# Performance work log

Measured on AMD Instinct MI355X. Metric: run time of the kernel, lower is better.

The kernel has to match this reference:

```python
import jax, jax.numpy as jnp
import numpy as np
import math
from jax.scipy.special import gammaln, logsumexp

N, D, K = 262144, 16, 64
K_TRUE = 32
TAU = 0.1
LOG2PI = math.log(2.0 * math.pi)


def setup_inputs() -> dict:
    key = jax.random.key(0)
    k0, k1, k2, k3, k4, k5 = jax.random.split(key, 6)
    # data locations, scaled so log(r_scale_met) > 0 (Gamma rate positivity, as in original init)
    met_locs = jax.random.normal(k0, (N, D), dtype=jnp.float32) * 20.0
    R = met_locs.max(0) - met_locs.min(0)  # per-dim range, diag of Ro
    r_scale = jnp.sqrt(jnp.sum(R ** 2)) / (2.0 * K_TRUE)
    mu = jax.random.normal(k1, (K, D), dtype=jnp.float32) * jnp.sqrt(R)[None, :]  # MVN(0, Ro)
    pi = jax.random.dirichlet(k2, jnp.full((K,), 1.0 / K, dtype=jnp.float32)).astype(jnp.float32)
    # log of Gamma(0.5, rate=0.5) sample; clipped for numerical safety of the setup draw
    lambda_mu = jnp.clip(jnp.log(jax.random.gamma(k3, 0.5, (D,)) / 0.5), -3.0, 3.0).astype(jnp.float32)
    b = jax.random.normal(k4, (K, D), dtype=jnp.float32)
    C = jnp.full((K,), jnp.log(r_scale), dtype=jnp.float32)
    r = jnp.full((K,), jnp.log(r_scale), dtype=jnp.float32)
    z = jax.random.normal(k5, (N, K), dtype=jnp.float32)
    return {"met_locs": met_locs, "mu": mu, "pi": pi, "lambda_mu": lambda_mu,
            "b": b, "C": C, "r": r, "z": z}


def reference(met_locs, mu, pi, lambda_mu, b, C, r, z):
    Df = float(D)
    R = met_locs.max(0) - met_locs.min(0)                      # diag of Ro
    c = 1.25 + (D - 1) / 4.0
    g = 0.25 + (D - 1) / 4.0
    G = c / (50.0 * g) * jnp.sqrt(jnp.sum(R ** 2))

    # ---- z_loss: Concrete prior on z_act + Concrete-weighted Gaussian mixture ----
    logz = jax.nn.log_softmax(z, axis=1)                       # log z_act, [N, K]
    logpi = jax.nn.log_softmax(pi)                             # [K]
    # isotropic Gaussian log N(x_m; mu_k, exp(r_k) I) without [N,K,D] intermediate
    sq = ((met_locs ** 2).sum(1, keepdims=True)
          - 2.0 * met_locs @ mu.T
          + (mu ** 2).sum(1)[None, :])                          # [N, K]
    logN = -0.5 * sq / jnp.exp(r)[None, :] - 0.5 * Df * (r + LOG2PI)[None, :]
    mix = logsumexp(logz + logN, axis=1)                       # log sum_k z_mk N_k(x_m)
    # Concrete (Gumbel-softmax) log-density at y = z_act with probs softmax(pi), temp TAU
    t = logpi[None, :] - TAU * logz                            # [N, K]
    con = (gammaln(float(K)) + (K - 1) * math.log(TAU)
           + jnp.sum(logpi) - (TAU + 1.0) * logz.sum(1)
           - K * logsumexp(t, axis=1))                          # [N]
    z_loss = -(con + mix).sum()

    # ---- pi_loss: Dirichlet(1/K) prior (up to const) ----
    pi_loss = -((1.0 / K - 1.0) * logpi).sum()

    # ---- mu_loss: MVN(b, Lambda Ro Lambda) with Lambda = diag(lambda_mu) ----
    var_mu = (lambda_mu ** 2) * R                              # diag of Bo, [D]
    mu_lp = (-0.5 * (((mu - b) ** 2) / var_mu[None, :]).sum(1)
             - 0.5 * jnp.log(var_mu).sum() - 0.5 * Df * LOG2PI)
    mu_loss = -mu_lp.sum()

    # ---- lambda_loss: Gamma(0.5, 0.5) on exp(lambda_mu) ----
    lam_lp = (0.5 * math.log(0.5) - gammaln(0.5)
              + (0.5 - 1.0) * lambda_mu - 0.5 * jnp.exp(lambda_mu))
    lambda_loss = -lam_lp.sum()

    # ---- b_loss: standard normal MVN ----
    b_loss = 0.5 * (b ** 2).sum() + 0.5 * K * Df * LOG2PI

    # ---- r_loss: Gamma(c, rate=C) on 1/exp(r) ----
    r_lp = c * jnp.log(C) + (c - 1.0) * (-r) - C * jnp.exp(-r) - gammaln(c)
    r_loss = -r_lp.sum()

    # ---- C_loss: Gamma(g, rate=G) on 1/exp(C) ----
    C_lp = g * jnp.log(G) + (g - 1.0) * (-C) - G * jnp.exp(-C) - gammaln(g)
    C_loss = -C_lp.sum()

    # forward sums in self.learn order: r, mu, z, pi, b, lambda, C
    return r_loss + mu_loss + z_loss + pi_loss + b_loss + lambda_loss + C_loss
```

## Files before the change

kernel.cpp:

```cpp
#include <hip/hip_runtime.h>
#include <math.h>

#define NROWS 262144
#define NBLK  1024
#define NTHR  256
#define LOG2PI_F 1.8378770664093453f
#define L2E_F   1.4426950408889634f
#define LN2_F   0.6931471805599453f

#define EXP2F(x) __builtin_amdgcn_exp2f(x)
#define LOG2F(x) __builtin_amdgcn_logf(x)

#define WS_ZS   1024
#define WS_MN   2048
#define WS_MX   18432
#define WS_CONS 34816

template<int CTRL>
__device__ __forceinline__ float dppf(float x){
  return __int_as_float(__builtin_amdgcn_update_dpp(0, __float_as_int(x), CTRL, 0xF, 0xF, true));
}
__device__ __forceinline__ float rl63(float x){
  return __int_as_float(__builtin_amdgcn_readlane(__float_as_int(x), 63));
}
__device__ __forceinline__ float wsum(float x){
  x += dppf<0x111>(x); x += dppf<0x112>(x); x += dppf<0x114>(x); x += dppf<0x118>(x);
  x += dppf<0x142>(x); x += dppf<0x143>(x);
  return rl63(x);
}

__global__ void setup_k(const float* __restrict__ mu, const float* __restrict__ pi,
                        const float* __restrict__ rr, float* __restrict__ ws){
  int k = threadIdx.x;
  float pik = pi[k], rk = rr[k];
  float mumu = 0.f;
  #pragma unroll
  for (int d = 0; d < 16; ++d){ float m = mu[k*16+d]; mumu = fmaf(m, m, mumu); }
  float lse_pi = __logf(wsum(__expf(pik)));
  float lpk = pik - lse_pi;
  float ir = __expf(-rk), Bk = -0.5f*ir;
  float Dk = fmaf(Bk, mumu, -8.f*(rk + LOG2PI_F));
  float* cons = ws + WS_CONS;
  cons[k*4+0] = __expf(lpk);
  cons[k*4+1] = ir*L2E_F;
  cons[k*4+2] = Dk*L2E_F;
  cons[k*4+3] = Bk*L2E_F;
}

__global__ __launch_bounds__(NTHR, 4)
void zmain(const float* __restrict__ met, const float* __restrict__ mu,
           const float* __restrict__ z, float* __restrict__ ws)
{
  __shared__ float zt[4][2112];
  const int tid = threadIdx.x, lane = tid & 63, wid = tid >> 6;
  const int bx = blockIdx.x;

  float pmn[4], pmx[4];
  #pragma unroll
  for (int j=0;j<4;++j){ pmn[j]=INFINITY; pmx[j]=-INFINITY; }
  {
    const float4* mb = (const float4*)(met + (size_t)bx*4096);
    #pragma unroll
    for (int i=0;i<4;++i){
      float4 v = mb[i*256 + tid];
      pmn[0]=fminf(pmn[0],v.x); pmx[0]=fmaxf(pmx[0],v.x);
      pmn[1]=fminf(pmn[1],v.y); pmx[1]=fmaxf(pmx[1],v.y);
      pmn[2]=fminf(pmn[2],v.z); pmx[2]=fmaxf(pmx[2],v.z);
      pmn[3]=fminf(pmn[3],v.w); pmx[3]=fmaxf(pmx[3],v.w);
    }
  }

  const int rbw = bx*256 + wid*64;
  const float4* xr = (const float4*)(met + (size_t)(rbw + lane)*16);
  float4 xa = xr[0], xb = xr[1], xc = xr[2], xd = xr[3];
  float xx = 0.f;
  xx=fmaf(xa.x,xa.x,xx); xx=fmaf(xa.y,xa.y,xx); xx=fmaf(xa.z,xa.z,xx); xx=fmaf(xa.w,xa.w,xx);
  xx=fmaf(xb.x,xb.x,xx); xx=fmaf(xb.y,xb.y,xx); xx=fmaf(xb.z,xb.z,xx); xx=fmaf(xb.w,xb.w,xx);
  xx=fmaf(xc.x,xc.x,xx); xx=fmaf(xc.y,xc.y,xx); xx=fmaf(xc.z,xc.z,xx); xx=fmaf(xc.w,xc.w,xx);
  xx=fmaf(xd.x,xd.x,xx); xx=fmaf(xd.y,xd.y,xx); xx=fmaf(xd.z,xd.z,xx); xx=fmaf(xd.w,xd.w,xx);

  const float4* z4 = (const float4*)z;
  const int g8 = lane >> 3, c8 = lane & 7;
  float4 sA[8], sB[8];
  #pragma unroll
  for (int j=0;j<8;++j) sA[j] = z4[(size_t)(rbw + j*8 + g8)*16 + c8];
  #pragma unroll
  for (int j=0;j<8;++j) sB[j] = z4[(size_t)(rbw + j*8 + g8)*16 + 8 + c8];
  #pragma unroll
  for (int j=0;j<8;++j){
    int b = (j*8+g8)*33 + c8*4;
    zt[wid][b]=sA[j].x; zt[wid][b+1]=sA[j].y; zt[wid][b+2]=sA[j].z; zt[wid][b+3]=sA[j].w;
  }

  const float4* cons4 = (const float4*)(ws + WS_CONS);
  const float4* mu4   = (const float4*)mu;

  float sez=0.f, seu=0.f, sea=0.f, m2=-1e30f, szA=0.f;

#define STEPK(K) { \
    float4 cc = cons4[K]; \
    float4 M0 = mu4[(K)*4+0], M1 = mu4[(K)*4+1], M2v = mu4[(K)*4+2], M3 = mu4[(K)*4+3]; \
    float zkv = zt[wid][lane*33 + ((K)&31)]; \
    float zk2 = zkv*L2E_F; \
    szA += zkv; \
    sez += EXP2F(zk2); \
    seu = fmaf(cc.x, EXP2F(-0.1f*zk2), seu); \
    float dt = 0.f; \
    dt=fmaf(xa.x,M0.x,dt); dt=fmaf(xa.y,M0.y,dt); dt=fmaf(xa.z,M0.z,dt); dt=fmaf(xa.w,M0.w,dt); \
    dt=fmaf(xb.x,M1.x,dt); dt=fmaf(xb.y,M1.y,dt); dt=fmaf(xb.z,M1.z,dt); dt=fmaf(xb.w,M1.w,dt); \
    dt=fmaf(xc.x,M2v.x,dt); dt=fmaf(xc.y,M2v.y,dt); dt=fmaf(xc.z,M2v.z,dt); dt=fmaf(xc.w,M2v.w,dt); \
    dt=fmaf(xd.x,M3.x,dt); dt=fmaf(xd.y,M3.y,dt); dt=fmaf(xd.z,M3.z,dt); dt=fmaf(xd.w,M3.w,dt); \
    float t1  = fmaf(cc.w, xx, zk2); \
    float av2 = fmaf(cc.y, dt, t1) + cc.z; \
    float d2 = av2 - m2; \
    float ee = EXP2F(-fabsf(d2)); \
    bool fl = d2 > 0.f; \
    sea = fmaf(sea, fl?ee:1.f, fl?1.f:ee); \
    m2 = fmaxf(m2, av2); }

  #pragma unroll 4
  for (int kk=0; kk<32; ++kk) STEPK(kk)

  #pragma unroll
  for (int j=0;j<8;++j){
    int b = (j*8+g8)*33 + c8*4;
    zt[wid][b]=sB[j].x; zt[wid][b+1]=sB[j].y; zt[wid][b+2]=sB[j].z; zt[wid][b+3]=sB[j].w;
  }
  #pragma unroll 4
  for (int kk=32; kk<64; ++kk) STEPK(kk)
#undef STEPK

  float l2sez = LOG2F(sez), l2seu = LOG2F(seu), l2sea = LOG2F(sea);
  float accA = LN2_F * (fmaf(63.f, l2sez, m2 + l2sea) - 64.f*l2seu);

  __syncthreads();
  float* scr = &zt[0][0];
  float wa = wsum(accA), wz = wsum(szA);
  if (lane == 0){ scr[2112 + wid] = wa; scr[2120 + wid] = wz; }
  #pragma unroll
  for (int j=0;j<4;++j){
    int d = (4*tid + j) & 15;
    scr[       d*66 + (tid>>2)] = pmn[j];
    scr[1056 + d*66 + (tid>>2)] = pmx[j];
  }
  __syncthreads();
  if (tid == 0){
    ws[bx]         = scr[2112]+scr[2113]+scr[2114]+scr[2115];
    ws[WS_ZS + bx] = scr[2120]+scr[2121]+scr[2122]+scr[2123];
  }
  if (tid < 16){
    float mnv = INFINITY, mxv = -INFINITY;
    for (int c2=0;c2<64;++c2){
      mnv = fminf(mnv, scr[tid*66+c2]);
      mxv = fmaxf(mxv, scr[1056+tid*66+c2]);
    }
    ws[WS_MN + bx*16 + tid] = mnv;
    ws[WS_MX + bx*16 + tid] = mxv;
  }
}

__global__ __launch_bounds__(NTHR)
void fin_k(const float* __restrict__ mu, const float* __restrict__ pi,
           const float* __restrict__ lam, const float* __restrict__ bp,
           const float* __restrict__ Cv,  const float* __restrict__ rr,
           const float* __restrict__ ws,  float* __restrict__ out,
           float cgam, float lamconst, float lg_c, float lg_g)
{
  __shared__ double sda[NTHR], sdz[NTHR];
  __shared__ float smn[16][66], smx[16][66];
  __shared__ float Rfin[16], vars[16];
  const int tid = threadIdx.x;

  {
    const float4* wa4 = (const float4*)ws;
    const float4* wz4 = (const float4*)(ws + WS_ZS);
    float4 a = wa4[tid], zz = wz4[tid];
    sda[tid] = (double)a.x + (double)a.y + (double)a.z + (double)a.w;
    sdz[tid] = (double)zz.x + (double)zz.y + (double)zz.z + (double)zz.w;
  }
  float pmn[4], pmx[4];
  #pragma unroll
  for (int j=0;j<4;++j){ pmn[j]=INFINITY; pmx[j]=-INFINITY; }
  {
    const float4* mn4 = (const float4*)(ws + WS_MN);
    const float4* mx4 = (const float4*)(ws + WS_MX);
    #pragma unroll
    for (int i=0;i<16;++i){
      float4 v = mn4[i*256 + tid];
      pmn[0]=fminf(pmn[0],v.x); pmn[1]=fminf(pmn[1],v.y);
      pmn[2]=fminf(pmn[2],v.z); pmn[3]=fminf(pmn[3],v.w);
      float4 w = mx4[i*256 + tid];
      pmx[0]=fmaxf(pmx[0],w.x); pmx[1]=fmaxf(pmx[1],w.y);
      pmx[2]=fmaxf(pmx[2],w.z); pmx[3]=fmaxf(pmx[3],w.w);
    }
  }
  #pragma unroll
  for (int j=0;j<4;++j){
    int d = (4*tid + j) & 15;
    smn[d][tid>>2] = pmn[j];
    smx[d][tid>>2] = pmx[j];
  }
  __syncthreads();
  for (int s = NTHR/2; s > 0; s >>= 1){
    if (tid < s){ sda[tid] += sda[tid+s]; sdz[tid] += sdz[tid+s]; }
    __syncthreads();
  }
  if (tid < 16){
    float mnv = INFINITY, mxv = -INFINITY;
    for (int c2=0;c2<64;++c2){ mnv = fminf(mnv, smn[tid][c2]); mxv = fmaxf(mxv, smx[tid][c2]); }
    float Rd = mxv - mnv;
    Rfin[tid] = Rd;
    float l = lam[tid];
    vars[tid] = l*l*Rd;
  }
  __syncthreads();

  if (tid < 64){
    int kk = tid;
    float sumR2 = 0.f;
    #pragma unroll
    for (int dd = 0; dd < 16; ++dd) sumR2 = fmaf(Rfin[dd], Rfin[dd], sumR2);
    float G = 0.025f * sqrtf(sumR2);

    float pik2 = pi[kk];
    float sp   = wsum(pik2);
    float lse2 = __logf(wsum(__expf(pik2)));
    float slogpi = sp - 64.f*lse2;

    float qsum = 0.f, slv = 0.f, bb = 0.f;
    #pragma unroll
    for (int dd = 0; dd < 16; ++dd){
      float df = mu[kk*16+dd] - bp[kk*16+dd];
      qsum += df*df / vars[dd];
      slv  += __logf(vars[dd]);
      float bv = bp[kk*16+dd];
      bb = fmaf(bv, bv, bb);
    }
    float mu_term = 0.5f*qsum + 0.5f*slv + 8.0f*LOG2PI_F;
    float rk2 = rr[kk], Ck = Cv[kk];
    float r_lp = 5.f*__logf(Ck) - 4.f*rk2 - Ck*__expf(-rk2) - lg_c;
    float C_lp = 4.f*__logf(G)  - 3.f*Ck  - G*__expf(-Ck)  - lg_g;
    float lam_term = 0.f;
    if (kk < 16){ float l = lam[kk]; lam_term = lamconst - 0.5f*l - 0.5f*__expf(l); }

    float per = mu_term + 0.5f*bb - r_lp - C_lp - lam_term;
    float persum = wsum(per);

    if (kk == 0){
      double zpart = sda[0] + 262144.0*(double)(cgam + slogpi) - 1.1*sdz[0];
      double tot = (double)persum
                 + (1.0 - 1.0/64.0)*(double)slogpi
                 + 512.0*(double)LOG2PI_F
                 - zpart;
      out[0] = (float)tot;
    }
  }
}

extern "C" void kernel_launch(void* const* d_in, const int* in_sizes, int n_in,
                              void* d_out, int out_size, void* d_ws, size_t ws_size,
                              hipStream_t stream) {
  const float* met = (const float*)d_in[0];
  const float* mu  = (const float*)d_in[1];
  const float* pi  = (const float*)d_in[2];
  const float* lam = (const float*)d_in[3];
  const float* bpp = (const float*)d_in[4];
  const float* Cv  = (const float*)d_in[5];
  const float* rr  = (const float*)d_in[6];
  const float* zz  = (const float*)d_in[7];
  float* out = (float*)d_out;
  float* ws  = (float*)d_ws;

  float cgam     = (float)(lgamma(64.0) + 63.0*log(0.1));
  float lamconst = (float)(0.5*log(0.5) - lgamma(0.5));
  float lg_c     = (float)lgamma(5.0);
  float lg_g     = (float)lgamma(4.0);

  setup_k<<<dim3(1), dim3(64), 0, stream>>>(mu, pi, rr, ws);
  zmain<<<dim3(NBLK), dim3(NTHR), 0, stream>>>(met, mu, zz, ws);
  fin_k<<<dim3(1), dim3(NTHR), 0, stream>>>(mu, pi, lam, bpp, Cv, rr, ws, out,
                                            cgam, lamconst, lg_c, lg_g);
}
```

Baseline: 131.5 us.

## Split K across wave pairs with direct z loads and LDS merge

Each row is now handled by two waves, each covering half of the 64 mixture components. Each wave reads its z values directly as float4 from its own row, replacing the LDS transpose staging. The partial max, sum and log-sum-exp states are merged through shared memory using a rescaled log-sum-exp combine. The block count doubles, launch bounds target higher occupancy, and the final reduction reads twice as many partials. This trades less per-thread serial work and no z transpose for uncoalesced per-row z loads and an extra barrier and merge step.

```diff
diff --git a/kernel.cpp b/kernel.cpp
--- a/kernel.cpp
+++ b/kernel.cpp
@@ -2,7 +2,7 @@
 #include <math.h>
 
 #define NROWS 262144
-#define NBLK  1024
+#define NBLK  2048
 #define NTHR  256
 #define LOG2PI_F 1.8378770664093453f
 #define L2E_F   1.4426950408889634f
@@ -11,10 +11,10 @@
 #define EXP2F(x) __builtin_amdgcn_exp2f(x)
 #define LOG2F(x) __builtin_amdgcn_logf(x)
 
-#define WS_ZS   1024
-#define WS_MN   2048
-#define WS_MX   18432
-#define WS_CONS 34816
+#define WS_ZS   2048
+#define WS_MN   4096
+#define WS_MX   36864
+#define WS_CONS 69632
 
 template<int CTRL>
 __device__ __forceinline__ float dppf(float x){
@@ -47,21 +47,24 @@
   cons[k*4+3] = Bk*L2E_F;
 }
 
-__global__ __launch_bounds__(NTHR, 4)
+__global__ __launch_bounds__(NTHR, 8)
 void zmain(const float* __restrict__ met, const float* __restrict__ mu,
            const float* __restrict__ z, float* __restrict__ ws)
 {
-  __shared__ float zt[4][2112];
+  __shared__ float mrg[2][64][6];
+  __shared__ float scr[2116];
   const int tid = threadIdx.x, lane = tid & 63, wid = tid >> 6;
+  const int pair = wid >> 1, kh = wid & 1;
   const int bx = blockIdx.x;
+  const int r = bx*128 + pair*64 + lane;
 
   float pmn[4], pmx[4];
   #pragma unroll
   for (int j=0;j<4;++j){ pmn[j]=INFINITY; pmx[j]=-INFINITY; }
   {
-    const float4* mb = (const float4*)(met + (size_t)bx*4096);
-    #pragma unroll
-    for (int i=0;i<4;++i){
+    const float4* mb = (const float4*)(met + (size_t)bx*2048);
+    #pragma unroll
+    for (int i=0;i<2;++i){
       float4 v = mb[i*256 + tid];
       pmn[0]=fminf(pmn[0],v.x); pmx[0]=fmaxf(pmx[0],v.x);
       pmn[1]=fminf(pmn[1],v.y); pmx[1]=fmaxf(pmx[1],v.y);
@@ -70,8 +73,7 @@
     }
   }
 
-  const int rbw = bx*256 + wid*64;
-  const float4* xr = (const float4*)(met + (size_t)(rbw + lane)*16);
+  const float4* xr = (const float4*)(met + (size_t)r*16);
   float4 xa = xr[0], xb = xr[1], xc = xr[2], xd = xr[3];
   float xx = 0.f;
   xx=fmaf(xa.x,xa.x,xx); xx=fmaf(xa.y,xa.y,xx); xx=fmaf(xa.z,xa.z,xx); xx=fmaf(xa.w,xa.w,xx);
@@ -79,30 +81,17 @@
   xx=fmaf(xc.x,xc.x,xx); xx=fmaf(xc.y,xc.y,xx); xx=fmaf(xc.z,xc.z,xx); xx=fmaf(xc.w,xc.w,xx);
   xx=fmaf(xd.x,xd.x,xx); xx=fmaf(xd.y,xd.y,xx); xx=fmaf(xd.z,xd.z,xx); xx=fmaf(xd.w,xd.w,xx);
 
-  const float4* z4 = (const float4*)z;
-  const int g8 = lane >> 3, c8 = lane & 7;
-  float4 sA[8], sB[8];
-  #pragma unroll
-  for (int j=0;j<8;++j) sA[j] = z4[(size_t)(rbw + j*8 + g8)*16 + c8];
-  #pragma unroll
-  for (int j=0;j<8;++j) sB[j] = z4[(size_t)(rbw + j*8 + g8)*16 + 8 + c8];
-  #pragma unroll
-  for (int j=0;j<8;++j){
-    int b = (j*8+g8)*33 + c8*4;
-    zt[wid][b]=sA[j].x; zt[wid][b+1]=sA[j].y; zt[wid][b+2]=sA[j].z; zt[wid][b+3]=sA[j].w;
-  }
-
-  const float4* cons4 = (const float4*)(ws + WS_CONS);
-  const float4* mu4   = (const float4*)mu;
+  const float4* cons4 = (const float4*)(ws + WS_CONS) + kh*32;
+  const float4* mu4   = (const float4*)mu + kh*128;
+  const float4* zrow  = (const float4*)z + (size_t)r*16 + kh*8;
 
   float sez=0.f, seu=0.f, sea=0.f, m2=-1e30f, szA=0.f;
 
-#define STEPK(K) { \
-    float4 cc = cons4[K]; \
-    float4 M0 = mu4[(K)*4+0], M1 = mu4[(K)*4+1], M2v = mu4[(K)*4+2], M3 = mu4[(K)*4+3]; \
-    float zkv = zt[wid][lane*33 + ((K)&31)]; \
-    float zk2 = zkv*L2E_F; \
-    szA += zkv; \
+#define STEPK(ZV, KK) { \
+    float4 cc = cons4[KK]; \
+    float4 M0 = mu4[(KK)*4+0], M1 = mu4[(KK)*4+1], M2v = mu4[(KK)*4+2], M3 = mu4[(KK)*4+3]; \
+    float zk2 = (ZV)*L2E_F; \
+    szA += (ZV); \
     sez += EXP2F(zk2); \
     seu = fmaf(cc.x, EXP2F(-0.1f*zk2), seu); \
     float dt = 0.f; \
@@ -118,25 +107,34 @@
     sea = fmaf(sea, fl?ee:1.f, fl?1.f:ee); \
     m2 = fmaxf(m2, av2); }
 
-  #pragma unroll 4
-  for (int kk=0; kk<32; ++kk) STEPK(kk)
-
-  #pragma unroll
-  for (int j=0;j<8;++j){
-    int b = (j*8+g8)*33 + c8*4;
-    zt[wid][b]=sB[j].x; zt[wid][b+1]=sB[j].y; zt[wid][b+2]=sB[j].z; zt[wid][b+3]=sB[j].w;
-  }
-  #pragma unroll 4
-  for (int kk=32; kk<64; ++kk) STEPK(kk)
+  #pragma unroll
+  for (int g=0; g<8; ++g){
+    float4 zq = zrow[g];
+    STEPK(zq.x, g*4+0)
+    STEPK(zq.y, g*4+1)
+    STEPK(zq.z, g*4+2)
+    STEPK(zq.w, g*4+3)
+  }
 #undef STEPK
 
-  float l2sez = LOG2F(sez), l2seu = LOG2F(seu), l2sea = LOG2F(sea);
-  float accA = LN2_F * (fmaf(63.f, l2sez, m2 + l2sea) - 64.f*l2seu);
-
-  __syncthreads();
-  float* scr = &zt[0][0];
-  float wa = wsum(accA), wz = wsum(szA);
-  if (lane == 0){ scr[2112 + wid] = wa; scr[2120 + wid] = wz; }
+  if (kh == 1){
+    mrg[pair][lane][0]=m2; mrg[pair][lane][1]=sez; mrg[pair][lane][2]=seu;
+    mrg[pair][lane][3]=sea; mrg[pair][lane][4]=szA;
+  }
+  __syncthreads();
+  float accA = 0.f, szT = 0.f;
+  if (kh == 0){
+    float m1 = mrg[pair][lane][0], sz1 = mrg[pair][lane][1], su1 = mrg[pair][lane][2];
+    float sa1 = mrg[pair][lane][3], zz1 = mrg[pair][lane][4];
+    float m = fmaxf(m2, m1);
+    float seaT = fmaf(sea, EXP2F(m2 - m), sa1*EXP2F(m1 - m));
+    float sezT = sez + sz1, seuT = seu + su1;
+    szT = szA + zz1;
+    accA = LN2_F * (fmaf(63.f, LOG2F(sezT), m + LOG2F(seaT)) - 64.f*LOG2F(seuT));
+  }
+
+  float wa = wsum(accA), wz = wsum(szT);
+  if (kh == 0 && lane == 0){ scr[2112 + pair] = wa; scr[2114 + pair] = wz; }
   #pragma unroll
   for (int j=0;j<4;++j){
     int d = (4*tid + j) & 15;
@@ -145,8 +143,8 @@
   }
   __syncthreads();
   if (tid == 0){
-    ws[bx]         = scr[2112]+scr[2113]+scr[2114]+scr[2115];
-    ws[WS_ZS + bx] = scr[2120]+scr[2121]+scr[2122]+scr[2123];
+    ws[bx]         = scr[2112] + scr[2113];
+    ws[WS_ZS + bx] = scr[2114] + scr[2115];
   }
   if (tid < 16){
     float mnv = INFINITY, mxv = -INFINITY;
@@ -174,9 +172,12 @@
   {
     const float4* wa4 = (const float4*)ws;
     const float4* wz4 = (const float4*)(ws + WS_ZS);
-    float4 a = wa4[tid], zz = wz4[tid];
-    sda[tid] = (double)a.x + (double)a.y + (double)a.z + (double)a.w;
-    sdz[tid] = (double)zz.x + (double)zz.y + (double)zz.z + (double)zz.w;
+    float4 a0 = wa4[tid], a1 = wa4[256 + tid];
+    float4 z0 = wz4[tid], z1 = wz4[256 + tid];
+    sda[tid] = (double)a0.x+(double)a0.y+(double)a0.z+(double)a0.w
+             + (double)a1.x+(double)a1.y+(double)a1.z+(double)a1.w;
+    sdz[tid] = (double)z0.x+(double)z0.y+(double)z0.z+(double)z0.w
+             + (double)z1.x+(double)z1.y+(double)z1.z+(double)z1.w;
   }
   float pmn[4], pmx[4];
   #pragma unroll
@@ -185,7 +186,7 @@
     const float4* mn4 = (const float4*)(ws + WS_MN);
     const float4* mx4 = (const float4*)(ws + WS_MX);
     #pragma unroll
-    for (int i=0;i<16;++i){
+    for (int i=0;i<32;++i){
       float4 v = mn4[i*256 + tid];
       pmn[0]=fminf(pmn[0],v.x); pmn[1]=fminf(pmn[1],v.y);
       pmn[2]=fminf(pmn[2],v.z); pmn[3]=fminf(pmn[3],v.w);
```

Result: slower. 309.6 us (+135.4%).

## Stage z in 16-column chunks with prefetch and raise occupancy target

Applied to the files above, without the earlier changes.

The z tile is now staged through shared memory in four 16-column chunks instead of two 32-column halves. The next chunk's global loads are issued before computing on the current chunk, so load latency overlaps with the exp/dot-product work. Shared memory per block drops from about 33KB to about 17KB, and launch bounds now ask for 8 waves per SIMD instead of 4. This frees registers and LDS for more resident blocks, but the tighter register budget could cause spills.

```diff
diff --git a/kernel.cpp b/kernel.cpp
--- a/kernel.cpp
+++ b/kernel.cpp
@@ -47,13 +47,14 @@
   cons[k*4+3] = Bk*L2E_F;
 }
 
-__global__ __launch_bounds__(NTHR, 4)
+__global__ __launch_bounds__(NTHR, 8)
 void zmain(const float* __restrict__ met, const float* __restrict__ mu,
            const float* __restrict__ z, float* __restrict__ ws)
 {
-  __shared__ float zt[4][2112];
+  __shared__ float smem[4352];
   const int tid = threadIdx.x, lane = tid & 63, wid = tid >> 6;
   const int bx = blockIdx.x;
+  float* zt = smem + wid*1088;
 
   float pmn[4], pmx[4];
   #pragma unroll
@@ -70,8 +71,8 @@
     }
   }
 
-  const int rbw = bx*256 + wid*64;
-  const float4* xr = (const float4*)(met + (size_t)(rbw + lane)*16);
+  const int rw0 = bx*256 + wid*64;
+  const float4* xr = (const float4*)(met + (size_t)(rw0 + lane)*16);
   float4 xa = xr[0], xb = xr[1], xc = xr[2], xd = xr[3];
   float xx = 0.f;
   xx=fmaf(xa.x,xa.x,xx); xx=fmaf(xa.y,xa.y,xx); xx=fmaf(xa.z,xa.z,xx); xx=fmaf(xa.w,xa.w,xx);
@@ -80,27 +81,30 @@
   xx=fmaf(xd.x,xd.x,xx); xx=fmaf(xd.y,xd.y,xx); xx=fmaf(xd.z,xd.z,xx); xx=fmaf(xd.w,xd.w,xx);
 
   const float4* z4 = (const float4*)z;
-  const int g8 = lane >> 3, c8 = lane & 7;
-  float4 sA[8], sB[8];
-  #pragma unroll
-  for (int j=0;j<8;++j) sA[j] = z4[(size_t)(rbw + j*8 + g8)*16 + c8];
-  #pragma unroll
-  for (int j=0;j<8;++j) sB[j] = z4[(size_t)(rbw + j*8 + g8)*16 + 8 + c8];
-  #pragma unroll
-  for (int j=0;j<8;++j){
-    int b = (j*8+g8)*33 + c8*4;
-    zt[wid][b]=sA[j].x; zt[wid][b+1]=sA[j].y; zt[wid][b+2]=sA[j].z; zt[wid][b+3]=sA[j].w;
-  }
-
+  const int rsub = lane >> 2, kq = lane & 3;
   const float4* cons4 = (const float4*)(ws + WS_CONS);
   const float4* mu4   = (const float4*)mu;
 
   float sez=0.f, seu=0.f, sea=0.f, m2=-1e30f, szA=0.f;
+  float4 pf0, pf1, pf2, pf3;
+
+#define LOADC(C) { \
+    pf0 = z4[(size_t)(rw0 +  0 + rsub)*16 + (C)*4 + kq]; \
+    pf1 = z4[(size_t)(rw0 + 16 + rsub)*16 + (C)*4 + kq]; \
+    pf2 = z4[(size_t)(rw0 + 32 + rsub)*16 + (C)*4 + kq]; \
+    pf3 = z4[(size_t)(rw0 + 48 + rsub)*16 + (C)*4 + kq]; }
+
+#define STORC() { \
+    int b = rsub*17 + kq*4; \
+    zt[b]=pf0.x; zt[b+1]=pf0.y; zt[b+2]=pf0.z; zt[b+3]=pf0.w; b += 272; \
+    zt[b]=pf1.x; zt[b+1]=pf1.y; zt[b+2]=pf1.z; zt[b+3]=pf1.w; b += 272; \
+    zt[b]=pf2.x; zt[b+1]=pf2.y; zt[b+2]=pf2.z; zt[b+3]=pf2.w; b += 272; \
+    zt[b]=pf3.x; zt[b+1]=pf3.y; zt[b+2]=pf3.z; zt[b+3]=pf3.w; }
 
 #define STEPK(K) { \
     float4 cc = cons4[K]; \
     float4 M0 = mu4[(K)*4+0], M1 = mu4[(K)*4+1], M2v = mu4[(K)*4+2], M3 = mu4[(K)*4+3]; \
-    float zkv = zt[wid][lane*33 + ((K)&31)]; \
+    float zkv = zt[lane*17 + ((K)&15)]; \
     float zk2 = zkv*L2E_F; \
     szA += zkv; \
     sez += EXP2F(zk2); \
@@ -118,25 +122,26 @@
     sea = fmaf(sea, fl?ee:1.f, fl?1.f:ee); \
     m2 = fmaxf(m2, av2); }
 
-  #pragma unroll 4
-  for (int kk=0; kk<32; ++kk) STEPK(kk)
-
-  #pragma unroll
-  for (int j=0;j<8;++j){
-    int b = (j*8+g8)*33 + c8*4;
-    zt[wid][b]=sB[j].x; zt[wid][b+1]=sB[j].y; zt[wid][b+2]=sB[j].z; zt[wid][b+3]=sB[j].w;
-  }
-  #pragma unroll 4
-  for (int kk=32; kk<64; ++kk) STEPK(kk)
+  LOADC(0)
+  #pragma unroll
+  for (int c = 0; c < 4; ++c){
+    STORC()
+    if (c == 0) LOADC(1)
+    else if (c == 1) LOADC(2)
+    else if (c == 2) LOADC(3)
+    #pragma unroll
+    for (int kk = 0; kk < 16; ++kk) STEPK(c*16 + kk)
+  }
 #undef STEPK
-
-  float l2sez = LOG2F(sez), l2seu = LOG2F(seu), l2sea = LOG2F(sea);
-  float accA = LN2_F * (fmaf(63.f, l2sez, m2 + l2sea) - 64.f*l2seu);
-
-  __syncthreads();
-  float* scr = &zt[0][0];
+#undef STORC
+#undef LOADC
+
+  float accA = LN2_F * (fmaf(63.f, LOG2F(sez), m2 + LOG2F(sea)) - 64.f*LOG2F(seu));
+
+  __syncthreads();
+  float* scr = smem;
   float wa = wsum(accA), wz = wsum(szA);
-  if (lane == 0){ scr[2112 + wid] = wa; scr[2120 + wid] = wz; }
+  if (lane == 0){ scr[2112 + wid] = wa; scr[2116 + wid] = wz; }
   #pragma unroll
   for (int j=0;j<4;++j){
     int d = (4*tid + j) & 15;
@@ -146,7 +151,7 @@
   __syncthreads();
   if (tid == 0){
     ws[bx]         = scr[2112]+scr[2113]+scr[2114]+scr[2115];
-    ws[WS_ZS + bx] = scr[2120]+scr[2121]+scr[2122]+scr[2123];
+    ws[WS_ZS + bx] = scr[2116]+scr[2117]+scr[2118]+scr[2119];
   }
   if (tid < 16){
     float mnv = INFINITY, mxv = -INFINITY;
```

Result: slower. 156.9 us (+19.3%).
